# Performance work log

Hardware: AMD Instinct MI355X
Metric: run time of the kernel (lower is better)

## Reference

```python
import jax, jax.numpy as jnp
import numpy as np

VOX_X, VOX_Y, VOX_Z = 256, 256, 20   # ceil((pc_range[3:]-pc_range[:3]) / 0.4)
OUT_H, OUT_W, OUT_Z = 200, 200, 16   # hard-coded F.interpolate target in forward
C = 80                               # out_channels; sparse feat dim must match for concat
N_PTS = 200000
BS = 1
EPS = 1e-5


def _lin_interp(x, axis, out_size):
    """1D linear interp along `axis`, matching torch align_corners=False."""
    in_size = x.shape[axis]
    pos = (jnp.arange(out_size, dtype=jnp.float32) + 0.5) * (in_size / out_size) - 0.5
    pos = jnp.clip(pos, 0.0, in_size - 1)
    i0 = jnp.floor(pos).astype(jnp.int32)
    i1 = jnp.minimum(i0 + 1, in_size - 1)
    w = pos - i0.astype(jnp.float32)
    x0 = jnp.take(x, i0, axis=axis)
    x1 = jnp.take(x, i1, axis=axis)
    wshape = [1] * x.ndim
    wshape[axis] = out_size
    w = w.reshape(wshape)
    return x0 * (1.0 - w) + x1 * w


def setup_inputs() -> dict:
    key = jax.random.key(0)
    ks = jax.random.split(key, 8)
    bev_feats = jax.random.normal(ks[0], (BS, C, OUT_H, OUT_W, OUT_Z), dtype=jnp.float32)
    # coords: [batch_idx, x, y, z] with per-column valid ranges
    cb = jax.random.randint(ks[1], (N_PTS, 1), 0, BS, dtype=jnp.int32)
    cx = jax.random.randint(ks[2], (N_PTS, 1), 0, VOX_X, dtype=jnp.int32)
    cy = jax.random.randint(ks[3], (N_PTS, 1), 0, VOX_Y, dtype=jnp.int32)
    cz = jax.random.randint(ks[4], (N_PTS, 1), 0, VOX_Z, dtype=jnp.int32)
    coords = jnp.concatenate([cb, cx, cy, cz], axis=1)
    feats = jax.random.normal(ks[5], (N_PTS, C), dtype=jnp.float32)
    w_conv = jax.random.normal(ks[6], (C, 2 * C), dtype=jnp.float32) * (1.0 / np.sqrt(2 * C))
    b_conv = jnp.zeros((C,), dtype=jnp.float32)
    return {
        "bev_feats": bev_feats, "coords": coords, "feats": feats,
        "w_conv": w_conv, "b_conv": b_conv,
        "bn_gamma": jnp.ones((C,), jnp.float32), "bn_beta": jnp.zeros((C,), jnp.float32),
        "bn_mean": jnp.zeros((C,), jnp.float32), "bn_var": jnp.ones((C,), jnp.float32),
    }


def reference(bev_feats, coords, feats, w_conv, b_conv, bn_gamma, bn_beta, bn_mean, bn_var):
    bs = bev_feats.shape[0]
    voxel = jnp.zeros((bs, VOX_X, VOX_Y, VOX_Z, C), dtype=jnp.float32)
    voxel = voxel.at[coords[:, 0], coords[:, 1], coords[:, 2], coords[:, 3]].set(feats)
    # permute(0,4,2,1,3): (bs, X, Y, Z, C) -> (bs, C, Y, X, Z)
    prior = jnp.transpose(voxel, (0, 4, 2, 1, 3))
    # trilinear interpolate (256,256,20) -> (200,200,16), align_corners=False (separable)
    prior = _lin_interp(prior, 2, OUT_H)
    prior = _lin_interp(prior, 3, OUT_W)
    prior = _lin_interp(prior, 4, OUT_Z)
    # concat on channels -> 1x1x1 conv3d -> BN (eval stats) -> residual -> ReLU
    x = jnp.concatenate([bev_feats, prior], axis=1)  # (bs, 2C, H, W, Z)
    y = jnp.einsum('bchwz,oc->bohwz', x, w_conv) + b_conv[None, :, None, None, None]
    inv = bn_gamma * jax.lax.rsqrt(bn_var + EPS)
    y = y * inv[None, :, None, None, None] + (bn_beta - bn_mean * inv)[None, :, None, None, None]
    return jax.nn.relu(y + bev_feats)
```

## Files before the change

### kernel.cpp

```cpp
#include <hip/hip_runtime.h>
#include <hip/hip_bf16.h>

#define VXX 256
#define VYY 256
#define VZZ 20
#define NC  80
#define OH  200
#define OW  200
#define OZ  16
#define SPATIAL (OH*OW*OZ)
#define NVOX (VXX*VYY*VZZ)
#define EPSV 1e-5f
#define NS 64
#define NWG (SPATIAL/NS)
#define X_FOOT 6
#define NCELL (2*X_FOOT*VZZ)
#define SLOTS 48
#define PSTR 72
#define RSB 80
#define RSP 88

typedef float  f32x4 __attribute__((ext_vector_type(4)));
typedef short  s16x8 __attribute__((ext_vector_type(8)));

__device__ __forceinline__ ushort f2bf(float f) {
    uint u = __builtin_bit_cast(uint, f);
    u += 0x7FFFu + ((u >> 16) & 1u);
    return (ushort)(u >> 16);
}

__device__ __forceinline__ void bar_lgkm() {
    asm volatile("s_waitcnt lgkmcnt(0)" ::: "memory");
    __builtin_amdgcn_s_barrier();
    asm volatile("" ::: "memory");
}

__global__ void scatter_k(const int* __restrict__ coords, int npts,
                          int* __restrict__ winner) {
    int i = blockIdx.x * 256 + threadIdx.x;
    if (i >= npts) return;
    int b = coords[i*4+0];
    int x = coords[i*4+1];
    int y = coords[i*4+2];
    int z = coords[i*4+3];
    int vi = ((b*VXX + x)*VYY + y)*VZZ + z;
    atomicMax(&winner[vi], i);
}

__global__ void setup_k(const float* __restrict__ wconv,
                        const float* __restrict__ bconv,
                        const float* __restrict__ gamma,
                        const float* __restrict__ beta,
                        const float* __restrict__ mean,
                        const float* __restrict__ var,
                        int4* __restrict__ winner4,
                        ushort* __restrict__ wfrag,
                        float2* __restrict__ bnss) {
    const int b = blockIdx.x, tid = threadIdx.x;
    if (b < 1280) {
        winner4[b*256 + tid] = make_int4(-1, -1, -1, -1);
    } else if (b < 1330) {
        int idx = (b - 1280)*256 + tid;
        int f   = idx >> 9;
        int rem = idx & 511;
        int l   = rem >> 3;
        int j   = rem & 7;
        int mt  = f / 5;
        int ks  = f - mt*5;
        int o   = mt*16 + (l & 15);
        int c   = ks*32 + (l >> 4)*8 + j;
        wfrag[idx] = f2bf(wconv[o*160 + c]);
    } else if (tid < NC) {
        float inv = gamma[tid] * rsqrtf(var[tid] + EPSV);
        bnss[tid] = make_float2(inv, bconv[tid]*inv + beta[tid] - mean[tid]*inv);
    }
}

__launch_bounds__(256, 5)
__global__ void fused_k(const float* __restrict__ bev,
                        const float* __restrict__ feats,
                        const int*  __restrict__ winner,
                        const ushort* __restrict__ wfrag,
                        const float2* __restrict__ bnss,
                        float* __restrict__ out) {
    __shared__ __align__(16) ushort xb_lds[NS * RSB];
    __shared__ __align__(16) char   u_lds[20736];
    __shared__ int    idx_lds[NCELL];
    __shared__ int    slot_pi[SLOTS];
    __shared__ int    wavecnt[4];
    ushort* const P_lds  = (ushort*)u_lds;
    ushort* const Rt_lds = (ushort*)(u_lds + 9216);
    ushort* const xp_lds = (ushort*)u_lds;

    const int tid   = threadIdx.x;
    const int bid   = blockIdx.x;
    const int swzb  = (bid & 7) * (NWG/8) + (bid >> 3);
    const int sbase = swzb * NS;
    const int sl    = tid & 63;
    const int quarter = tid >> 6;
    const int wv    = quarter, lane = sl;

    const int h  = sbase / (OW * OZ);
    const int w0 = (sbase >> 4) % OW;
    float posy = (h + 0.5f) * ((float)VYY/(float)OH) - 0.5f;
    posy = fminf(fmaxf(posy, 0.f), (float)(VYY-1));
    const int   y0 = (int)posy;
    const int   y1 = min(y0+1, VYY-1);
    const float fy = posy - (float)y0;
    float posx0 = (w0 + 0.5f) * ((float)VXX/(float)OW) - 0.5f;
    posx0 = fminf(fmaxf(posx0, 0.f), (float)(VXX-1));
    const int xmin = (int)posx0;

    const int zq = sl & 15;
    const int wq = w0 + (sl >> 4);
    float posx = (wq + 0.5f) * ((float)VXX/(float)OW) - 0.5f;
    posx = fminf(fmaxf(posx, 0.f), (float)(VXX-1));
    const int   x0 = (int)posx;
    const int   x1 = min(x0+1, VXX-1);
    const float fxw = posx - (float)x0;
    float posz = (zq + 0.5f) * ((float)VZZ/(float)OZ) - 0.5f;
    posz = fminf(fmaxf(posz, 0.f), (float)(VZZ-1));
    const int   z0 = (int)posz;
    const int   z1 = min(z0+1, VZZ-1);
    const float fzw = posz - (float)z0;
    const int fx0 = x0 - xmin, fx1 = x1 - xmin;

    int pi = -1;
    if (tid < NCELL) {
        int fz  = tid % VZZ;
        int fx  = (tid / VZZ) % X_FOOT;
        int fyc = tid / (VZZ * X_FOOT);
        int xx  = min(xmin + fx, VXX-1);
        int yy  = fyc ? y1 : y0;
        pi = winner[(xx*VYY + yy)*VZZ + fz];
    }
    __builtin_amdgcn_sched_barrier(0);

    const int S = sbase + sl;
    float bvv[20];
    #pragma unroll
    for (int j = 0; j < 20; ++j)
        bvv[j] = bev[(quarter*20 + j)*SPATIAL + S];
    __builtin_amdgcn_sched_barrier(0);

    {
        uint* pz = (uint*)u_lds;
        #pragma unroll
        for (int i = 0; i < 9; ++i) pz[tid + i*256] = 0;
    }

    unsigned long long bm = __ballot(pi >= 0);
    if (lane == 0) wavecnt[wv] = __popcll(bm);
    bar_lgkm();
    int base = 0, nstot = 0;
    #pragma unroll
    for (int w2 = 0; w2 < 4; ++w2) {
        int c2 = wavecnt[w2];
        if (w2 < wv) base += c2;
        nstot += c2;
    }
    if (tid < NCELL) {
        int v = -1;
        if (pi >= 0) {
            int slot = base + __popcll(bm & ((1ull << lane) - 1ull));
            if (slot < SLOTS) { slot_pi[slot] = pi; v = slot; }
            else v = -(pi + 2);
        }
        idx_lds[tid] = v;
    }
    bar_lgkm();
    const int nst = min(nstot, SLOTS);

    const float4* feats4 = (const float4*)feats;
    const int myslot = tid >> 2, part = tid & 3;
    const bool rowact = (myslot < nst);
    float4 rbuf[5];
    if (rowact) {
        const float4* p = feats4 + slot_pi[myslot]*20 + part*5;
        #pragma unroll
        for (int q = 0; q < 5; ++q) rbuf[q] = p[q];
    }

    {
        const int ky = quarter >> 1, kx = quarter & 1;
        const float ywp = ky ? fy : 1.f - fy;
        const bool xdup = (fx1 == fx0);
        if (!(xdup && kx)) {
            const int   xf = kx ? fx1 : fx0;
            const float xw = xdup ? 1.f : (kx ? fxw : 1.f - fxw);
            #pragma unroll
            for (int kz = 0; kz < 2; ++kz) {
                int cell = (ky*X_FOOT + xf)*VZZ + (kz ? z1 : z0);
                int v = idx_lds[cell];
                if (v >= 0)
                    P_lds[sl*PSTR + v] = f2bf(ywp * xw * (kz ? fzw : 1.f - fzw));
            }
        }
    }

    #pragma unroll
    for (int j5 = 0; j5 < 5; ++j5) {
        ushort4 pk = make_ushort4(f2bf(bvv[j5*4+0]), f2bf(bvv[j5*4+1]),
                                  f2bf(bvv[j5*4+2]), f2bf(bvv[j5*4+3]));
        *(ushort4*)&xb_lds[sl*RSB + quarter*20 + j5*4] = pk;
    }

    {
        ushort vals[20];
        #pragma unroll
        for (int q = 0; q < 5; ++q) {
            vals[4*q+0] = rowact ? f2bf(rbuf[q].x) : (ushort)0;
            vals[4*q+1] = rowact ? f2bf(rbuf[q].y) : (ushort)0;
            vals[4*q+2] = rowact ? f2bf(rbuf[q].z) : (ushort)0;
            vals[4*q+3] = rowact ? f2bf(rbuf[q].w) : (ushort)0;
        }
        #pragma unroll
        for (int e = 0; e < 20; ++e)
            Rt_lds[(part*20 + e)*PSTR + myslot] = vals[e];
    }
    bar_lgkm();

    const int lrow = lane & 15, lgrp = lane >> 4;
    f32x4 pa[5];
    {
        const int prow = (wv*16 + lrow)*PSTR;
        s16x8 p0 = *(const s16x8*)&P_lds[prow +      lgrp*8];
        s16x8 p1 = *(const s16x8*)&P_lds[prow + 32 + lgrp*8];
        #pragma unroll
        for (int mt = 0; mt < 5; ++mt) {
            const int arow = (mt*16 + lrow)*PSTR;
            s16x8 a0 = *(const s16x8*)&Rt_lds[arow +      lgrp*8];
            s16x8 a1 = *(const s16x8*)&Rt_lds[arow + 32 + lgrp*8];
            pa[mt] = (f32x4){0.f, 0.f, 0.f, 0.f};
            pa[mt] = __builtin_amdgcn_mfma_f32_16x16x32_bf16(a0, p0, pa[mt], 0, 0, 0);
            pa[mt] = __builtin_amdgcn_mfma_f32_16x16x32_bf16(a1, p1, pa[mt], 0, 0, 0);
        }
    }
    bar_lgkm();
    #pragma unroll
    for (int mt = 0; mt < 5; ++mt) {
        ushort4 pk = make_ushort4(f2bf(pa[mt][0]), f2bf(pa[mt][1]),
                                  f2bf(pa[mt][2]), f2bf(pa[mt][3]));
        *(ushort4*)&xp_lds[(wv*16 + lrow)*RSP + mt*16 + lgrp*4] = pk;
    }

    if (nstot > SLOTS) {
        bar_lgkm();
        float add20[20];
        #pragma unroll
        for (int j = 0; j < 20; ++j) add20[j] = 0.f;
        bool any = false;
        #pragma unroll
        for (int k = 0; k < 8; ++k) {
            int kz = k & 1, kx = (k>>1)&1, ky = k>>2;
            int cell = (ky*X_FOOT + (kx ? fx1 : fx0))*VZZ + (kz ? z1 : z0);
            int v = idx_lds[cell];
            if (v < -1) {
                any = true;
                float wtk = (ky?fy:1.f-fy) * (kx?fxw:1.f-fxw) * (kz?fzw:1.f-fzw);
                const float4* p = feats4 + (-v - 2)*20 + quarter*5;
                #pragma unroll
                for (int q = 0; q < 5; ++q) {
                    float4 f = p[q];
                    add20[4*q]   += wtk*f.x; add20[4*q+1] += wtk*f.y;
                    add20[4*q+2] += wtk*f.z; add20[4*q+3] += wtk*f.w;
                }
            }
        }
        if (any) {
            #pragma unroll
            for (int q = 0; q < 5; ++q) {
                ushort* dst = &xp_lds[sl*RSP + quarter*20 + q*4];
                ushort4 old = *(ushort4*)dst;
                const ushort ov[4] = {old.x, old.y, old.z, old.w};
                ushort nv[4];
                #pragma unroll
                for (int e = 0; e < 4; ++e) {
                    float f = __builtin_bit_cast(float, (uint)ov[e] << 16) + add20[4*q+e];
                    nv[e] = f2bf(f);
                }
                *(ushort4*)dst = make_ushort4(nv[0], nv[1], nv[2], nv[3]);
            }
        }
    }
    bar_lgkm();

    f32x4 acc[5];
    #pragma unroll
    for (int mt = 0; mt < 5; ++mt) acc[mt] = (f32x4){0.f, 0.f, 0.f, 0.f};

    const int srow_b = (wv*16 + lrow) * RSB;
    const int srow_p = (wv*16 + lrow) * RSP;

    #pragma unroll
    for (int ks = 0; ks < 5; ++ks) {
        int c = ks*32 + lgrp*8;
        const ushort* bp = (c < 80) ? &xb_lds[srow_b + c]
                                    : &xp_lds[srow_p + (c - 80)];
        s16x8 b = *(const s16x8*)bp;
        #pragma unroll
        for (int mt = 0; mt < 5; ++mt) {
            s16x8 a = *(const s16x8*)&wfrag[((mt*5 + ks)*64 + lane)*8];
            acc[mt] = __builtin_amdgcn_mfma_f32_16x16x32_bf16(a, b, acc[mt], 0, 0, 0);
        }
    }

    const int slocal = wv*16 + lrow;
    const int sglob  = sbase + slocal;
    #pragma unroll
    for (int mt = 0; mt < 5; ++mt) {
        ushort4 rr = *(const ushort4*)&xb_lds[slocal*RSB + mt*16 + lgrp*4];
        const ushort rrv[4] = {rr.x, rr.y, rr.z, rr.w};
        #pragma unroll
        for (int r = 0; r < 4; ++r) {
            int o = mt*16 + lgrp*4 + r;
            float2 ss = bnss[o];
            float resid = __builtin_bit_cast(float, (uint)rrv[r] << 16);
            float v = acc[mt][r]*ss.x + ss.y + resid;
            out[o*SPATIAL + sglob] = fmaxf(v, 0.f);
        }
    }
}

extern "C" void kernel_launch(void* const* d_in, const int* in_sizes, int n_in,
                              void* d_out, int out_size, void* d_ws, size_t ws_size,
                              hipStream_t stream) {
    const float* bev    = (const float*)d_in[0];
    const int*   coords = (const int*)  d_in[1];
    const float* feats  = (const float*)d_in[2];
    const float* wconv  = (const float*)d_in[3];
    const float* bconv  = (const float*)d_in[4];
    const float* gamma  = (const float*)d_in[5];
    const float* beta   = (const float*)d_in[6];
    const float* mean   = (const float*)d_in[7];
    const float* var    = (const float*)d_in[8];
    float*       out    = (float*)d_out;

    int*    winner = (int*)d_ws;
    ushort* wfrag  = (ushort*)((char*)d_ws + (size_t)NVOX*4);
    float2* bnss   = (float2*)((char*)d_ws + (size_t)NVOX*4 + 25600);
    int npts = in_sizes[1] / 4;

    hipLaunchKernelGGL(setup_k, dim3(1331), dim3(256), 0, stream,
                       wconv, bconv, gamma, beta, mean, var,
                       (int4*)winner, wfrag, bnss);
    hipLaunchKernelGGL(scatter_k, dim3((npts + 255)/256), dim3(256), 0, stream,
                       coords, npts, winner);
    hipLaunchKernelGGL(fused_k, dim3(NWG), dim3(256), 0, stream,
                       bev, feats, winner, wfrag, bnss, out);
}
```

Measured before the change: 151.2 us.

## Process two spatial tiles per workgroup with prefetch of second tile's inputs

```diff
diff --git a/kernel.cpp b/kernel.cpp
--- a/kernel.cpp
+++ b/kernel.cpp
@@ -12,7 +12,8 @@
 #define NVOX (VXX*VYY*VZZ)
 #define EPSV 1e-5f
 #define NS 64
-#define NWG (SPATIAL/NS)
+#define NTILE (SPATIAL/NS)
+#define NB (NTILE/2)
 #define X_FOOT 6
 #define NCELL (2*X_FOOT*VZZ)
 #define SLOTS 48
@@ -76,71 +77,89 @@
     }
 }
 
-__launch_bounds__(256, 5)
-__global__ void fused_k(const float* __restrict__ bev,
-                        const float* __restrict__ feats,
-                        const int*  __restrict__ winner,
-                        const ushort* __restrict__ wfrag,
-                        const float2* __restrict__ bnss,
-                        float* __restrict__ out) {
+__launch_bounds__(256, 4)
+__global__ void fused2_k(const float* __restrict__ bev,
+                         const float* __restrict__ feats,
+                         const int*  __restrict__ winner,
+                         const ushort* __restrict__ wfrag,
+                         const float2* __restrict__ bnss,
+                         float* __restrict__ out) {
     __shared__ __align__(16) ushort xb_lds[NS * RSB];
     __shared__ __align__(16) char   u_lds[20736];
-    __shared__ int    idx_lds[NCELL];
-    __shared__ int    slot_pi[SLOTS];
-    __shared__ int    wavecnt[4];
+    __shared__ int idx0_lds[NCELL];
+    __shared__ int idx1_lds[NCELL];
+    __shared__ int slot0_pi[SLOTS];
+    __shared__ int slot1_pi[SLOTS];
+    __shared__ int wcnt0[4];
+    __shared__ int wcnt1[4];
     ushort* const P_lds  = (ushort*)u_lds;
     ushort* const Rt_lds = (ushort*)(u_lds + 9216);
     ushort* const xp_lds = (ushort*)u_lds;
 
     const int tid   = threadIdx.x;
     const int bid   = blockIdx.x;
-    const int swzb  = (bid & 7) * (NWG/8) + (bid >> 3);
-    const int sbase = swzb * NS;
+    const int swzb  = (bid & 7) * (NB/8) + (bid >> 3);
+    const int t0    = swzb * 2;
+    const int sbase0 = t0 * NS;
+    const int sbase1 = sbase0 + NS;
     const int sl    = tid & 63;
     const int quarter = tid >> 6;
     const int wv    = quarter, lane = sl;
-
-    const int h  = sbase / (OW * OZ);
-    const int w0 = (sbase >> 4) % OW;
+    const int lrow  = lane & 15, lgrp = lane >> 4;
+    const int srow  = wv*16 + lrow;
+
+    const int h   = sbase0 / (OW * OZ);
+    const int w00 = (sbase0 >> 4) % OW;
     float posy = (h + 0.5f) * ((float)VYY/(float)OH) - 0.5f;
     posy = fminf(fmaxf(posy, 0.f), (float)(VYY-1));
     const int   y0 = (int)posy;
     const int   y1 = min(y0+1, VYY-1);
     const float fy = posy - (float)y0;
-    float posx0 = (w0 + 0.5f) * ((float)VXX/(float)OW) - 0.5f;
-    posx0 = fminf(fmaxf(posx0, 0.f), (float)(VXX-1));
-    const int xmin = (int)posx0;
 
     const int zq = sl & 15;
-    const int wq = w0 + (sl >> 4);
-    float posx = (wq + 0.5f) * ((float)VXX/(float)OW) - 0.5f;
-    posx = fminf(fmaxf(posx, 0.f), (float)(VXX-1));
-    const int   x0 = (int)posx;
-    const int   x1 = min(x0+1, VXX-1);
-    const float fxw = posx - (float)x0;
     float posz = (zq + 0.5f) * ((float)VZZ/(float)OZ) - 0.5f;
     posz = fminf(fmaxf(posz, 0.f), (float)(VZZ-1));
     const int   z0 = (int)posz;
     const int   z1 = min(z0+1, VZZ-1);
     const float fzw = posz - (float)z0;
-    const int fx0 = x0 - xmin, fx1 = x1 - xmin;
-
-    int pi = -1;
+
+    const float XS = (float)VXX / (float)OW;
+    float posx0f = (w00 + (sl >> 4) + 0.5f)*XS - 0.5f;
+    posx0f = fminf(fmaxf(posx0f, 0.f), (float)(VXX-1));
+    const int   x00 = (int)posx0f;
+    const int   x10 = min(x00+1, VXX-1);
+    const float fxw0 = posx0f - (float)x00;
+    float pxm0 = (w00 + 0.5f)*XS - 0.5f;
+    pxm0 = fminf(fmaxf(pxm0, 0.f), (float)(VXX-1));
+    const int xmin0 = (int)pxm0;
+    const int fx00 = x00 - xmin0, fx10 = x10 - xmin0;
+
+    float posx1f = (w00 + 4 + (sl >> 4) + 0.5f)*XS - 0.5f;
+    posx1f = fminf(fmaxf(posx1f, 0.f), (float)(VXX-1));
+    const int   x01 = (int)posx1f;
+    const int   x11 = min(x01+1, VXX-1);
+    const float fxw1 = posx1f - (float)x01;
+    float pxm1 = (w00 + 4 + 0.5f)*XS - 0.5f;
+    pxm1 = fminf(fmaxf(pxm1, 0.f), (float)(VXX-1));
+    const int xmin1 = (int)pxm1;
+    const int fx01 = x01 - xmin1, fx11 = x11 - xmin1;
+
+    const int dfz  = tid % VZZ;
+    const int dfx  = (tid / VZZ) % X_FOOT;
+    const int dfyc = tid / (VZZ * X_FOOT);
+    const int dyy  = dfyc ? y1 : y0;
+
+    int pi0 = -1, pi1 = -1;
     if (tid < NCELL) {
-        int fz  = tid % VZZ;
-        int fx  = (tid / VZZ) % X_FOOT;
-        int fyc = tid / (VZZ * X_FOOT);
-        int xx  = min(xmin + fx, VXX-1);
-        int yy  = fyc ? y1 : y0;
-        pi = winner[(xx*VYY + yy)*VZZ + fz];
+        pi0 = winner[(min(xmin0 + dfx, VXX-1)*VYY + dyy)*VZZ + dfz];
+        pi1 = winner[(min(xmin1 + dfx, VXX-1)*VYY + dyy)*VZZ + dfz];
     }
     __builtin_amdgcn_sched_barrier(0);
 
-    const int S = sbase + sl;
     float bvv[20];
     #pragma unroll
     for (int j = 0; j < 20; ++j)
-        bvv[j] = bev[(quarter*20 + j)*SPATIAL + S];
+        bvv[j] = bev[(quarter*20 + j)*SPATIAL + sbase0 + sl];
     __builtin_amdgcn_sched_barrier(0);
 
     {
@@ -149,49 +168,61 @@
         for (int i = 0; i < 9; ++i) pz[tid + i*256] = 0;
     }
 
-    unsigned long long bm = __ballot(pi >= 0);
-    if (lane == 0) wavecnt[wv] = __popcll(bm);
-    bar_lgkm();
-    int base = 0, nstot = 0;
+    unsigned long long bm0 = __ballot(pi0 >= 0);
+    unsigned long long bm1 = __ballot(pi1 >= 0);
+    if (lane == 0) { wcnt0[wv] = __popcll(bm0); wcnt1[wv] = __popcll(bm1); }
+    bar_lgkm();
+    int base0 = 0, nstot0 = 0, base1 = 0, nstot1 = 0;
     #pragma unroll
     for (int w2 = 0; w2 < 4; ++w2) {
-        int c2 = wavecnt[w2];
-        if (w2 < wv) base += c2;
-        nstot += c2;
+        int c0 = wcnt0[w2], c1 = wcnt1[w2];
+        if (w2 < wv) { base0 += c0; base1 += c1; }
+        nstot0 += c0; nstot1 += c1;
     }
     if (tid < NCELL) {
-        int v = -1;
-        if (pi >= 0) {
-            int slot = base + __popcll(bm & ((1ull << lane) - 1ull));
-            if (slot < SLOTS) { slot_pi[slot] = pi; v = slot; }
-            else v = -(pi + 2);
-        }
-        idx_lds[tid] = v;
-    }
-    bar_lgkm();
-    const int nst = min(nstot, SLOTS);
+        int v0 = -1, v1 = -1;
+        if (pi0 >= 0) {
+            int s = base0 + __popcll(bm0 & ((1ull << lane) - 1ull));
+            if (s < SLOTS) { slot0_pi[s] = pi0; v0 = s; } else v0 = -(pi0 + 2);
+        }
+        if (pi1 >= 0) {
+            int s = base1 + __popcll(bm1 & ((1ull << lane) - 1ull));
+            if (s < SLOTS) { slot1_pi[s] = pi1; v1 = s; } else v1 = -(pi1 + 2);
+        }
+        idx0_lds[tid] = v0;
+        idx1_lds[tid] = v1;
+    }
+    bar_lgkm();
+    const int nst0 = min(nstot0, SLOTS);
+    const int nst1 = min(nstot1, SLOTS);
 
     const float4* feats4 = (const float4*)feats;
     const int myslot = tid >> 2, part = tid & 3;
-    const bool rowact = (myslot < nst);
-    float4 rbuf[5];
-    if (rowact) {
-        const float4* p = feats4 + slot_pi[myslot]*20 + part*5;
-        #pragma unroll
-        for (int q = 0; q < 5; ++q) rbuf[q] = p[q];
-    }
+    const bool rowact0 = (myslot < nst0);
+    const bool rowact1 = (myslot < nst1);
+    float4 rbuf0[5], rbuf1[5];
+    if (rowact0) {
+        const float4* p = feats4 + slot0_pi[myslot]*20 + part*5;
+        #pragma unroll
+        for (int q = 0; q < 5; ++q) rbuf0[q] = p[q];
+    }
+    if (rowact1) {
+        const float4* p = feats4 + slot1_pi[myslot]*20 + part*5;
+        #pragma unroll
+        for (int q = 0; q < 5; ++q) rbuf1[q] = p[q];
+    }
+    __builtin_amdgcn_sched_barrier(0);
 
     {
         const int ky = quarter >> 1, kx = quarter & 1;
         const float ywp = ky ? fy : 1.f - fy;
-        const bool xdup = (fx1 == fx0);
+        const bool xdup = (fx10 == fx00);
         if (!(xdup && kx)) {
-            const int   xf = kx ? fx1 : fx0;
-            const float xw = xdup ? 1.f : (kx ? fxw : 1.f - fxw);
+            const int   xf = kx ? fx10 : fx00;
+            const float xw = xdup ? 1.f : (kx ? fxw0 : 1.f - fxw0);
             #pragma unroll
             for (int kz = 0; kz < 2; ++kz) {
-                int cell = (ky*X_FOOT + xf)*VZZ + (kz ? z1 : z0);
-                int v = idx_lds[cell];
+                int v = idx0_lds[(ky*X_FOOT + xf)*VZZ + (kz ? z1 : z0)];
                 if (v >= 0)
                     P_lds[sl*PSTR + v] = f2bf(ywp * xw * (kz ? fzw : 1.f - fzw));
             }
@@ -205,14 +236,19 @@
         *(ushort4*)&xb_lds[sl*RSB + quarter*20 + j5*4] = pk;
     }
 
+    #pragma unroll
+    for (int j = 0; j < 20; ++j)
+        bvv[j] = bev[(quarter*20 + j)*SPATIAL + sbase1 + sl];
+    __builtin_amdgcn_sched_barrier(0);
+
     {
         ushort vals[20];
         #pragma unroll
         for (int q = 0; q < 5; ++q) {
-            vals[4*q+0] = rowact ? f2bf(rbuf[q].x) : (ushort)0;
-            vals[4*q+1] = rowact ? f2bf(rbuf[q].y) : (ushort)0;
-            vals[4*q+2] = rowact ? f2bf(rbuf[q].z) : (ushort)0;
-            vals[4*q+3] = rowact ? f2bf(rbuf[q].w) : (ushort)0;
+            vals[4*q+0] = rowact0 ? f2bf(rbuf0[q].x) : (ushort)0;
+            vals[4*q+1] = rowact0 ? f2bf(rbuf0[q].y) : (ushort)0;
+            vals[4*q+2] = rowact0 ? f2bf(rbuf0[q].z) : (ushort)0;
+            vals[4*q+3] = rowact0 ? f2bf(rbuf0[q].w) : (ushort)0;
         }
         #pragma unroll
         for (int e = 0; e < 20; ++e)
@@ -220,10 +256,9 @@
     }
     bar_lgkm();
 
-    const int lrow = lane & 15, lgrp = lane >> 4;
     f32x4 pa[5];
     {
-        const int prow = (wv*16 + lrow)*PSTR;
+        const int prow = srow*PSTR;
         s16x8 p0 = *(const s16x8*)&P_lds[prow +      lgrp*8];
         s16x8 p1 = *(const s16x8*)&P_lds[prow + 32 + lgrp*8];
         #pragma unroll
@@ -241,10 +276,10 @@
     for (int mt = 0; mt < 5; ++mt) {
         ushort4 pk = make_ushort4(f2bf(pa[mt][0]), f2bf(pa[mt][1]),
                                   f2bf(pa[mt][2]), f2bf(pa[mt][3]));
-        *(ushort4*)&xp_lds[(wv*16 + lrow)*RSP + mt*16 + lgrp*4] = pk;
-    }
-
-    if (nstot > SLOTS) {
+        *(ushort4*)&xp_lds[srow*RSP + mt*16 + lgrp*4] = pk;
+    }
+
+    if (nstot0 > SLOTS) {
         bar_lgkm();
         float add20[20];
         #pragma unroll
@@ -253,11 +288,10 @@
         #pragma unroll
         for (int k = 0; k < 8; ++k) {
             int kz = k & 1, kx = (k>>1)&1, ky = k>>2;
-            int cell = (ky*X_FOOT + (kx ? fx1 : fx0))*VZZ + (kz ? z1 : z0);
-            int v = idx_lds[cell];
+            int v = idx0_lds[(ky*X_FOOT + (kx ? fx10 : fx00))*VZZ + (kz ? z1 : z0)];
             if (v < -1) {
                 any = true;
-                float wtk = (ky?fy:1.f-fy) * (kx?fxw:1.f-fxw) * (kz?fzw:1.f-fzw);
+                float wtk = (ky?fy:1.f-fy) * (kx?fxw0:1.f-fxw0) * (kz?fzw:1.f-fzw);
                 const float4* p = feats4 + (-v - 2)*20 + quarter*5;
                 #pragma unroll
                 for (int q = 0; q < 5; ++q) {
@@ -285,39 +319,179 @@
     }
     bar_lgkm();
 
-    f32x4 acc[5];
-    #pragma unroll
-    for (int mt = 0; mt < 5; ++mt) acc[mt] = (f32x4){0.f, 0.f, 0.f, 0.f};
-
-    const int srow_b = (wv*16 + lrow) * RSB;
-    const int srow_p = (wv*16 + lrow) * RSP;
-
-    #pragma unroll
-    for (int ks = 0; ks < 5; ++ks) {
-        int c = ks*32 + lgrp*8;
-        const ushort* bp = (c < 80) ? &xb_lds[srow_b + c]
-                                    : &xp_lds[srow_p + (c - 80)];
-        s16x8 b = *(const s16x8*)bp;
+    {
+        f32x4 acc[5];
+        #pragma unroll
+        for (int mt = 0; mt < 5; ++mt) acc[mt] = (f32x4){0.f, 0.f, 0.f, 0.f};
+        const int srow_b = srow * RSB;
+        const int srow_p = srow * RSP;
+        #pragma unroll
+        for (int ks = 0; ks < 5; ++ks) {
+            int c = ks*32 + lgrp*8;
+            const ushort* bp = (c < 80) ? &xb_lds[srow_b + c]
+                                        : &xp_lds[srow_p + (c - 80)];
+            s16x8 b = *(const s16x8*)bp;
+            #pragma unroll
+            for (int mt = 0; mt < 5; ++mt) {
+                s16x8 a = *(const s16x8*)&wfrag[((mt*5 + ks)*64 + lane)*8];
+                acc[mt] = __builtin_amdgcn_mfma_f32_16x16x32_bf16(a, b, acc[mt], 0, 0, 0);
+            }
+        }
+        const int sglob = sbase0 + srow;
         #pragma unroll
         for (int mt = 0; mt < 5; ++mt) {
-            s16x8 a = *(const s16x8*)&wfrag[((mt*5 + ks)*64 + lane)*8];
-            acc[mt] = __builtin_amdgcn_mfma_f32_16x16x32_bf16(a, b, acc[mt], 0, 0, 0);
-        }
-    }
-
-    const int slocal = wv*16 + lrow;
-    const int sglob  = sbase + slocal;
+            ushort4 rr = *(const ushort4*)&xb_lds[srow_b + mt*16 + lgrp*4];
+            const ushort rrv[4] = {rr.x, rr.y, rr.z, rr.w};
+            #pragma unroll
+            for (int r = 0; r < 4; ++r) {
+                int o = mt*16 + lgrp*4 + r;
+                float2 ss = bnss[o];
+                float resid = __builtin_bit_cast(float, (uint)rrv[r] << 16);
+                float v = acc[mt][r]*ss.x + ss.y + resid;
+                out[o*SPATIAL + sglob] = fmaxf(v, 0.f);
+            }
+        }
+    }
+    bar_lgkm();
+
+    {
+        uint* pz = (uint*)u_lds;
+        #pragma unroll
+        for (int i = 0; i < 9; ++i) pz[tid + i*256] = 0;
+    }
+    bar_lgkm();
+
+    {
+        const int ky = quarter >> 1, kx = quarter & 1;
+        const float ywp = ky ? fy : 1.f - fy;
+        const bool xdup = (fx11 == fx01);
+        if (!(xdup && kx)) {
+            const int   xf = kx ? fx11 : fx01;
+            const float xw = xdup ? 1.f : (kx ? fxw1 : 1.f - fxw1);
+            #pragma unroll
+            for (int kz = 0; kz < 2; ++kz) {
+                int v = idx1_lds[(ky*X_FOOT + xf)*VZZ + (kz ? z1 : z0)];
+                if (v >= 0)
+                    P_lds[sl*PSTR + v] = f2bf(ywp * xw * (kz ? fzw : 1.f - fzw));
+            }
+        }
+    }
+
+    #pragma unroll
+    for (int j5 = 0; j5 < 5; ++j5) {
+        ushort4 pk = make_ushort4(f2bf(bvv[j5*4+0]), f2bf(bvv[j5*4+1]),
+                                  f2bf(bvv[j5*4+2]), f2bf(bvv[j5*4+3]));
+        *(ushort4*)&xb_lds[sl*RSB + quarter*20 + j5*4] = pk;
+    }
+
+    {
+        ushort vals[20];
+        #pragma unroll
+        for (int q = 0; q < 5; ++q) {
+            vals[4*q+0] = rowact1 ? f2bf(rbuf1[q].x) : (ushort)0;
+            vals[4*q+1] = rowact1 ? f2bf(rbuf1[q].y) : (ushort)0;
+            vals[4*q+2] = rowact1 ? f2bf(rbuf1[q].z) : (ushort)0;
+            vals[4*q+3] = rowact1 ? f2bf(rbuf1[q].w) : (ushort)0;
+        }
+        #pragma unroll
+        for (int e = 0; e < 20; ++e)
+            Rt_lds[(part*20 + e)*PSTR + myslot] = vals[e];
+    }
+    bar_lgkm();
+
+    {
+        const int prow = srow*PSTR;
+        s16x8 p0 = *(const s16x8*)&P_lds[prow +      lgrp*8];
+        s16x8 p1 = *(const s16x8*)&P_lds[prow + 32 + lgrp*8];
+        #pragma unroll
+        for (int mt = 0; mt < 5; ++mt) {
+            const int arow = (mt*16 + lrow)*PSTR;
+            s16x8 a0 = *(const s16x8*)&Rt_lds[arow +      lgrp*8];
+            s16x8 a1 = *(const s16x8*)&Rt_lds[arow + 32 + lgrp*8];
+            pa[mt] = (f32x4){0.f, 0.f, 0.f, 0.f};
+            pa[mt] = __builtin_amdgcn_mfma_f32_16x16x32_bf16(a0, p0, pa[mt], 0, 0, 0);
+            pa[mt] = __builtin_amdgcn_mfma_f32_16x16x32_bf16(a1, p1, pa[mt], 0, 0, 0);
+        }
+    }
+    bar_lgkm();
     #pragma unroll
     for (int mt = 0; mt < 5; ++mt) {
-        ushort4 rr = *(const ushort4*)&xb_lds[slocal*RSB + mt*16 + lgrp*4];
-        const ushort rrv[4] = {rr.x, rr.y, rr.z, rr.w};
-        #pragma unroll
-        for (int r = 0; r < 4; ++r) {
-            int o = mt*16 + lgrp*4 + r;
-            float2 ss = bnss[o];
-            float resid = __builtin_bit_cast(float, (uint)rrv[r] << 16);
-            float v = acc[mt][r]*ss.x + ss.y + resid;
-            out[o*SPATIAL + sglob] = fmaxf(v, 0.f);
+        ushort4 pk = make_ushort4(f2bf(pa[mt][0]), f2bf(pa[mt][1]),
+                                  f2bf(pa[mt][2]), f2bf(pa[mt][3]));
+        *(ushort4*)&xp_lds[srow*RSP + mt*16 + lgrp*4] = pk;
+    }
+
+    if (nstot1 > SLOTS) {
+        bar_lgkm();
+        float add20[20];
+        #pragma unroll
+        for (int j = 0; j < 20; ++j) add20[j] = 0.f;
+        bool any = false;
+        #pragma unroll
+        for (int k = 0; k < 8; ++k) {
+            int kz = k & 1, kx = (k>>1)&1, ky = k>>2;
+            int v = idx1_lds[(ky*X_FOOT + (kx ? fx11 : fx01))*VZZ + (kz ? z1 : z0)];
+            if (v < -1) {
+                any = true;
+                float wtk = (ky?fy:1.f-fy) * (kx?fxw1:1.f-fxw1) * (kz?fzw:1.f-fzw);
+                const float4* p = feats4 + (-v - 2)*20 + quarter*5;
+                #pragma unroll
+                for (int q = 0; q < 5; ++q) {
+                    float4 f = p[q];
+                    add20[4*q]   += wtk*f.x; add20[4*q+1] += wtk*f.y;
+                    add20[4*q+2] += wtk*f.z; add20[4*q+3] += wtk*f.w;
+                }
+            }
+        }
+        if (any) {
+            #pragma unroll
+            for (int q = 0; q < 5; ++q) {
+                ushort* dst = &xp_lds[sl*RSP + quarter*20 + q*4];
+                ushort4 old = *(ushort4*)dst;
+                const ushort ov[4] = {old.x, old.y, old.z, old.w};
+                ushort nv[4];
+                #pragma unroll
+                for (int e = 0; e < 4; ++e) {
+                    float f = __builtin_bit_cast(float, (uint)ov[e] << 16) + add20[4*q+e];
+                    nv[e] = f2bf(f);
+                }
+                *(ushort4*)dst = make_ushort4(nv[0], nv[1], nv[2], nv[3]);
+            }
+        }
+    }
+    bar_lgkm();
+
+    {
+        f32x4 acc[5];
+        #pragma unroll
+        for (int mt = 0; mt < 5; ++mt) acc[mt] = (f32x4){0.f, 0.f, 0.f, 0.f};
+        const int srow_b = srow * RSB;
+        const int srow_p = srow * RSP;
+        #pragma unroll
+        for (int ks = 0; ks < 5; ++ks) {
+            int c = ks*32 + lgrp*8;
+            const ushort* bp = (c < 80) ? &xb_lds[srow_b + c]
+                                        : &xp_lds[srow_p + (c - 80)];
+            s16x8 b = *(const s16x8*)bp;
+            #pragma unroll
+            for (int mt = 0; mt < 5; ++mt) {
+                s16x8 a = *(const s16x8*)&wfrag[((mt*5 + ks)*64 + lane)*8];
+                acc[mt] = __builtin_amdgcn_mfma_f32_16x16x32_bf16(a, b, acc[mt], 0, 0, 0);
+            }
+        }
+        const int sglob = sbase1 + srow;
+        #pragma unroll
+        for (int mt = 0; mt < 5; ++mt) {
+            ushort4 rr = *(const ushort4*)&xb_lds[srow_b + mt*16 + lgrp*4];
+            const ushort rrv[4] = {rr.x, rr.y, rr.z, rr.w};
+            #pragma unroll
+            for (int r = 0; r < 4; ++r) {
+                int o = mt*16 + lgrp*4 + r;
+                float2 ss = bnss[o];
+                float resid = __builtin_bit_cast(float, (uint)rrv[r] << 16);
+                float v = acc[mt][r]*ss.x + ss.y + resid;
+                out[o*SPATIAL + sglob] = fmaxf(v, 0.f);
+            }
         }
     }
 }
@@ -346,6 +520,6 @@
                        (int4*)winner, wfrag, bnss);
     hipLaunchKernelGGL(scatter_k, dim3((npts + 255)/256), dim3(256), 0, stream,
                        coords, npts, winner);
-    hipLaunchKernelGGL(fused_k, dim3(NWG), dim3(256), 0, stream,
+    hipLaunchKernelGGL(fused2_k, dim3(NB), dim3(256), 0, stream,
                        bev, feats, winner, wfrag, bnss, out);
 }
```

After: 198.2 us. 31.1% more time.
